# Kernel tuning notes

Measured on AMD Instinct MI355X. Metric: run time of the kernel, lower is better.

Reference implementation:

```python
import jax, jax.numpy as jnp
import numpy as np

GRID_SIZE = 5
SPLINE_ORDER = 3
GRID_RANGE = (-1.0, 1.0)
IN_FEATURES = 1024
OUT_FEATURES = 1024
NUM_BASIS = GRID_SIZE + SPLINE_ORDER  # 8
SCALE_BASE = 1.0
SCALE_SPLINE = 1.0

_h = (GRID_RANGE[1] - GRID_RANGE[0]) / GRID_SIZE
_GRID = np.linspace(GRID_RANGE[0] - SPLINE_ORDER * _h,
                    GRID_RANGE[1] + SPLINE_ORDER * _h,
                    GRID_SIZE + 2 * SPLINE_ORDER + 1).astype(np.float32)  # (12,)


def bspline_basis(x, grid):
    # x: (B, I)  ->  basis: (B, I, NUM_BASIS)
    x = jnp.clip(x, GRID_RANGE[0], GRID_RANGE[1])
    xg = x[..., None]                              # (B, I, 1)
    g = grid                                       # (G,) broadcasts over (B, I)
    basis = ((xg >= g[:-1]) & (xg < g[1:])).astype(x.dtype)  # (B, I, G-1)
    for k in range(1, SPLINE_ORDER + 1):
        left_den = g[k:-1] - g[:-(k + 1)]
        left_den = jnp.where(left_den == 0, jnp.ones_like(left_den), left_den)
        right_den = g[k + 1:] - g[1:-k]
        right_den = jnp.where(right_den == 0, jnp.ones_like(right_den), right_den)
        left = (xg - g[:-(k + 1)]) / left_den * basis[..., :-1]
        right = (g[k + 1:] - xg) / right_den * basis[..., 1:]
        basis = left + right
    return basis


def setup_inputs() -> dict:
    key = jax.random.key(0)
    k1, k2, k3 = jax.random.split(key, 3)
    x = jax.random.normal(k1, (8192, IN_FEATURES), dtype=jnp.float32)
    base_weight = jax.random.normal(k2, (OUT_FEATURES, IN_FEATURES), dtype=jnp.float32) * 0.03
    spline_weight = jax.random.normal(k3, (OUT_FEATURES, IN_FEATURES, NUM_BASIS), dtype=jnp.float32) * 0.03
    return {"x": x, "base_weight": base_weight, "spline_weight": spline_weight}


def reference(x, base_weight, spline_weight):
    grid = jnp.asarray(_GRID, dtype=x.dtype)
    # base branch: SiLU(x) @ W_base^T
    base_out = jax.nn.silu(x) @ base_weight.T              # (B, O)
    base_out = base_out * SCALE_BASE
    # spline branch: einsum over (in, basis)
    basis = bspline_basis(x, grid)                         # (B, I, K)
    spline_out = jnp.einsum('bik,oik->bo', basis, spline_weight)
    spline_out = spline_out * SCALE_SPLINE
    return base_out + spline_out
```

## Files before the change

kernel.cpp:

```cpp
#include <hip/hip_runtime.h>
#include <hip/hip_bf16.h>
#include <cstdint>


typedef short s16x8 __attribute__((ext_vector_type(8)));
typedef float f32x4 __attribute__((ext_vector_type(4)));

#define GK 9216
#define GN 1024
#define GI 1024
#define GM 8192

#define BS_BLK 32768
#define RP_BLK 4608

__device__ __forceinline__ void cp16(const __hip_bfloat16* g, __hip_bfloat16* l) {
  __builtin_amdgcn_global_load_lds((const __attribute__((address_space(1))) void*)g,
                                   (__attribute__((address_space(3))) void*)l, 16, 0, 0);
}

__device__ __forceinline__ uint32_t bfbits(float f) {
  __hip_bfloat16 h = __float2bfloat16(f);
  unsigned short us;
  __builtin_memcpy(&us, &h, 2);
  return (uint32_t)us;
}

__device__ __forceinline__ void basis4(float xv, int& jj, float& w0, float& w1,
                                       float& w2, float& w3) {
  float t = fminf(1.f, fmaxf(-1.f, xv));
  float us = (t + 1.f) * 2.5f;
  int j = (int)us;
  if (j > 4) j = 4;
  float u = us - (float)j;
  float u2 = u * u, u3 = u2 * u;
  float om = 1.f - u;
  jj = j;
  w0 = om * om * om * (1.f / 6.f);
  w1 = (3.f * u3 - 6.f * u2 + 4.f) * (1.f / 6.f);
  w2 = (-3.f * u3 + 3.f * u2 + 3.f * u + 1.f) * (1.f / 6.f);
  w3 = u3 * (1.f / 6.f);
}

__global__ void kan_prep_all(const float* __restrict__ x,
                             const float* __restrict__ baseW,
                             const float* __restrict__ splineW,
                             __hip_bfloat16* __restrict__ W2,
                             __hip_bfloat16* __restrict__ A) {
  int bid = blockIdx.x;
  if (bid < BS_BLK) {
    int t = bid * 256 + threadIdx.x;
    int b = t >> 10, i = t & 1023;
    float xv = x[t];

    float sl = xv / (1.f + __expf(-xv));
    A[(size_t)b * GK + 8192 + i] = __float2bfloat16(sl);

    int jj; float w0, w1, w2, w3;
    basis4(xv, jj, w0, w1, w2, w3);
    uint64_t W64 = (uint64_t)(bfbits(w0) | (bfbits(w1) << 16)) |
                   ((uint64_t)(bfbits(w2) | (bfbits(w3) << 16)) << 32);
    int sh = jj * 16;
    uint64_t lo = (jj < 4) ? (W64 << sh) : 0ull;
    uint64_t hi = (jj == 0) ? 0ull : (W64 >> (64 - sh));
    uint4 pk;
    pk.x = (uint32_t)lo;  pk.y = (uint32_t)(lo >> 32);
    pk.z = (uint32_t)hi;  pk.w = (uint32_t)(hi >> 32);
    *(uint4*)(A + (size_t)b * GK + (size_t)i * 8) = pk;
  } else {
    int t = (bid - BS_BLK) * 256 + threadIdx.x;
    int o = t / 1152;
    int c = (t - o * 1152) * 8;
    const float* src = (c < 8192) ? (splineW + (size_t)o * 8192 + c)
                                  : (baseW + (size_t)o * GI + (c - 8192));
    float4 v0 = ((const float4*)src)[0];
    float4 v1 = ((const float4*)src)[1];
    uint4 pk;
    pk.x = bfbits(v0.x) | (bfbits(v0.y) << 16);
    pk.y = bfbits(v0.z) | (bfbits(v0.w) << 16);
    pk.z = bfbits(v1.x) | (bfbits(v1.y) << 16);
    pk.w = bfbits(v1.z) | (bfbits(v1.w) << 16);
    *(uint4*)(W2 + (size_t)o * GK + c) = pk;
  }
}

__global__ __launch_bounds__(256) void kan_gemm(
    const __hip_bfloat16* __restrict__ A,
    const __hip_bfloat16* __restrict__ B,
    float* __restrict__ C) {
  __shared__ __align__(16) __hip_bfloat16 As[2][128 * 32];
  __shared__ __align__(16) __hip_bfloat16 Bs[2][128 * 32];
  const int tid = threadIdx.x;
  const int lane = tid & 63;
  const int wave = tid >> 6;
  const int wm = wave >> 1, wn = wave & 1;

  const int linear = blockIdx.y * 8 + blockIdx.x;
  const int rowBand = (linear & 7) * 8 + ((linear >> 3) & 7);
  const int colBand = linear >> 6;
  const int blockRow = rowBand * 128;
  const int blockCol = colBand * 128;

  const __hip_bfloat16* aPtr = A + (size_t)(blockRow + (tid >> 2)) * GK + (tid & 3) * 8;
  const __hip_bfloat16* bPtr = B + (size_t)(blockCol + (tid >> 2)) * GK + (tid & 3) * 8;
  __hip_bfloat16* ldsA0 = As[0] + wave * 512;
  __hip_bfloat16* ldsA1 = As[1] + wave * 512;
  __hip_bfloat16* ldsB0 = Bs[0] + wave * 512;
  __hip_bfloat16* ldsB1 = Bs[1] + wave * 512;

  f32x4 acc[4][4] = {};

  const int q = lane >> 4;
  const int r16 = lane & 15;
  const int aRow = wm * 64 + r16;
  const int bRow = wn * 64 + r16;

  for (int kt = 0; kt < GK / 64; ++kt) {
    cp16(aPtr, ldsA0);
    cp16(aPtr + (size_t)64 * GK, ldsA0 + 2048);
    cp16(aPtr + 32, ldsA1);
    cp16(aPtr + 32 + (size_t)64 * GK, ldsA1 + 2048);
    cp16(bPtr, ldsB0);
    cp16(bPtr + (size_t)64 * GK, ldsB0 + 2048);
    cp16(bPtr + 32, ldsB1);
    cp16(bPtr + 32 + (size_t)64 * GK, ldsB1 + 2048);
    aPtr += 64; bPtr += 64;
    __syncthreads();

#pragma unroll
    for (int s = 0; s < 2; ++s) {
      const s16x8* Af = (const s16x8*)As[s];
      const s16x8* Bf = (const s16x8*)Bs[s];
      s16x8 af[4], bfg[4];
#pragma unroll
      for (int tm = 0; tm < 4; ++tm) af[tm] = Af[(aRow + tm * 16) * 4 + q];
#pragma unroll
      for (int tn = 0; tn < 4; ++tn) bfg[tn] = Bf[(bRow + tn * 16) * 4 + q];
#pragma unroll
      for (int tm = 0; tm < 4; ++tm)
#pragma unroll
        for (int tn = 0; tn < 4; ++tn)
          acc[tm][tn] = __builtin_amdgcn_mfma_f32_16x16x32_bf16(
              af[tm], bfg[tn], acc[tm][tn], 0, 0, 0);
    }
    __syncthreads();
  }

  const int cRow0 = blockRow + wm * 64 + q * 4;
  const int cCol0 = blockCol + wn * 64 + r16;
#pragma unroll
  for (int tm = 0; tm < 4; ++tm)
#pragma unroll
    for (int tn = 0; tn < 4; ++tn) {
      int col = cCol0 + tn * 16;
#pragma unroll
      for (int r = 0; r < 4; ++r) {
        int row = cRow0 + tm * 16 + r;
        C[(size_t)row * GN + col] = acc[tm][tn][r];
      }
    }
}

__global__ void kan_naive(const float* __restrict__ x,
                          const float* __restrict__ bw,
                          const float* __restrict__ sw,
                          float* __restrict__ out) {
  int o = blockIdx.x * 256 + threadIdx.x;
  int b = blockIdx.y;
  float acc = 0.f;
  for (int i = 0; i < GI; ++i) {
    float xv = x[(size_t)b * GI + i];
    float sl = xv / (1.f + __expf(-xv));
    acc += sl * bw[(size_t)o * GI + i];
    int jj; float w0, w1, w2, w3;
    basis4(xv, jj, w0, w1, w2, w3);
    const float* swr = sw + ((size_t)o * GI + i) * 8 + jj;
    acc += w0 * swr[0] + w1 * swr[1] + w2 * swr[2] + w3 * swr[3];
  }
  out[(size_t)b * GN + o] = acc;
}

extern "C" void kernel_launch(void* const* d_in, const int* in_sizes, int n_in,
                              void* d_out, int out_size, void* d_ws, size_t ws_size,
                              hipStream_t stream) {
  const float* x  = (const float*)d_in[0];
  const float* bw = (const float*)d_in[1];
  const float* sw = (const float*)d_in[2];
  float* out = (float*)d_out;

  const size_t wBytes = (size_t)GK * GN * 2;
  const size_t aBytes = (size_t)GM * GK * 2;
  if (ws_size < wBytes + aBytes) {
    kan_naive<<<dim3(GN / 256, GM), 256, 0, stream>>>(x, bw, sw, out);
    return;
  }

  __hip_bfloat16* W2 = (__hip_bfloat16*)d_ws;
  __hip_bfloat16* Abuf = W2 + (size_t)GK * GN;

  kan_prep_all<<<BS_BLK + RP_BLK, 256, 0, stream>>>(x, bw, sw, W2, Abuf);
  kan_gemm<<<dim3(GN / 128, GM / 128), 256, 0, stream>>>(Abuf, W2, out);
}
```

Measured before the change: 290.0 us.

## Fuse prep and GEMM into one kernel with a global grid barrier

The separate preprocessing kernel (basis expansion, SiLU, weight conversion to bf16) is merged into the GEMM kernel. Each of the 512 GEMM blocks first prepares a slice of the activation and weight buffers, then waits at an atomic-counter grid barrier before running the matmul. This removes a kernel launch and its tail, but it relies on all 512 blocks being resident at once (launch_bounds 256,2), adds a memset, and makes the prep phase run with far fewer threads than before.

```diff
diff --git a/kernel.cpp b/kernel.cpp
--- a/kernel.cpp
+++ b/kernel.cpp
@@ -10,9 +10,7 @@
 #define GN 1024
 #define GI 1024
 #define GM 8192
-
-#define BS_BLK 32768
-#define RP_BLK 4608
+#define NBLOCKS 512u
 
 __device__ __forceinline__ void cp16(const __hip_bfloat16* g, __hip_bfloat16* l) {
   __builtin_amdgcn_global_load_lds((const __attribute__((address_space(1))) void*)g,
@@ -42,67 +40,96 @@
   w3 = u3 * (1.f / 6.f);
 }
 
-__global__ void kan_prep_all(const float* __restrict__ x,
-                             const float* __restrict__ baseW,
-                             const float* __restrict__ splineW,
-                             __hip_bfloat16* __restrict__ W2,
-                             __hip_bfloat16* __restrict__ A) {
-  int bid = blockIdx.x;
-  if (bid < BS_BLK) {
-    int t = bid * 256 + threadIdx.x;
-    int b = t >> 10, i = t & 1023;
-    float xv = x[t];
-
-    float sl = xv / (1.f + __expf(-xv));
-    A[(size_t)b * GK + 8192 + i] = __float2bfloat16(sl);
-
-    int jj; float w0, w1, w2, w3;
-    basis4(xv, jj, w0, w1, w2, w3);
-    uint64_t W64 = (uint64_t)(bfbits(w0) | (bfbits(w1) << 16)) |
-                   ((uint64_t)(bfbits(w2) | (bfbits(w3) << 16)) << 32);
-    int sh = jj * 16;
-    uint64_t lo = (jj < 4) ? (W64 << sh) : 0ull;
-    uint64_t hi = (jj == 0) ? 0ull : (W64 >> (64 - sh));
-    uint4 pk;
-    pk.x = (uint32_t)lo;  pk.y = (uint32_t)(lo >> 32);
-    pk.z = (uint32_t)hi;  pk.w = (uint32_t)(hi >> 32);
-    *(uint4*)(A + (size_t)b * GK + (size_t)i * 8) = pk;
-  } else {
-    int t = (bid - BS_BLK) * 256 + threadIdx.x;
-    int o = t / 1152;
-    int c = (t - o * 1152) * 8;
-    const float* src = (c < 8192) ? (splineW + (size_t)o * 8192 + c)
-                                  : (baseW + (size_t)o * GI + (c - 8192));
-    float4 v0 = ((const float4*)src)[0];
-    float4 v1 = ((const float4*)src)[1];
-    uint4 pk;
-    pk.x = bfbits(v0.x) | (bfbits(v0.y) << 16);
-    pk.y = bfbits(v0.z) | (bfbits(v0.w) << 16);
-    pk.z = bfbits(v1.x) | (bfbits(v1.y) << 16);
-    pk.w = bfbits(v1.z) | (bfbits(v1.w) << 16);
-    *(uint4*)(W2 + (size_t)o * GK + c) = pk;
-  }
-}
-
-__global__ __launch_bounds__(256) void kan_gemm(
-    const __hip_bfloat16* __restrict__ A,
-    const __hip_bfloat16* __restrict__ B,
-    float* __restrict__ C) {
+__device__ __forceinline__ uint4 basispack(float xv) {
+  int jj; float w0, w1, w2, w3;
+  basis4(xv, jj, w0, w1, w2, w3);
+  uint64_t W64 = (uint64_t)(bfbits(w0) | (bfbits(w1) << 16)) |
+                 ((uint64_t)(bfbits(w2) | (bfbits(w3) << 16)) << 32);
+  int sh = jj * 16;
+  uint64_t lo = (jj < 4) ? (W64 << sh) : 0ull;
+  uint64_t hi = (jj == 0) ? 0ull : (W64 >> (64 - sh));
+  uint4 pk;
+  pk.x = (uint32_t)lo;  pk.y = (uint32_t)(lo >> 32);
+  pk.z = (uint32_t)hi;  pk.w = (uint32_t)(hi >> 32);
+  return pk;
+}
+
+__global__ __launch_bounds__(256, 2) void kan_fused(
+    const float* __restrict__ x,
+    const float* __restrict__ baseW,
+    const float* __restrict__ splineW,
+    __hip_bfloat16* __restrict__ W2,
+    __hip_bfloat16* __restrict__ A,
+    float* __restrict__ C,
+    uint32_t* __restrict__ gate) {
   __shared__ __align__(16) __hip_bfloat16 As[2][128 * 32];
   __shared__ __align__(16) __hip_bfloat16 Bs[2][128 * 32];
   const int tid = threadIdx.x;
+
+  const int linear = blockIdx.y * 8 + blockIdx.x;
+  const int rowBand = (linear & 7) * 8 + ((linear >> 3) & 7);
+  const int colBand = linear >> 6;
+
+  {
+    const int rowStart = rowBand * 128 + colBand * 16;
+#pragma unroll 4
+    for (int it = 0; it < 16; ++it) {
+      int f = it * 1024 + tid * 4;
+      int b = rowStart + (f >> 10);
+      int i = f & 1023;
+      float4 xv = *(const float4*)(x + (size_t)b * GI + i);
+      uint4* bp = (uint4*)(A + (size_t)b * GK + (size_t)i * 8);
+      bp[0] = basispack(xv.x);
+      bp[1] = basispack(xv.y);
+      bp[2] = basispack(xv.z);
+      bp[3] = basispack(xv.w);
+      float s0 = xv.x / (1.f + __expf(-xv.x));
+      float s1 = xv.y / (1.f + __expf(-xv.y));
+      float s2 = xv.z / (1.f + __expf(-xv.z));
+      float s3 = xv.w / (1.f + __expf(-xv.w));
+      uint2 sp;
+      sp.x = bfbits(s0) | (bfbits(s1) << 16);
+      sp.y = bfbits(s2) | (bfbits(s3) << 16);
+      *(uint2*)(A + (size_t)b * GK + 8192 + i) = sp;
+    }
+  }
+
+  {
+#pragma unroll
+    for (int k = 0; k < 9; ++k) {
+      int chunk = k * 256 + tid;
+      int o = linear * 2 + (chunk / 1152);
+      int c = (chunk % 1152) * 8;
+      const float* src = (c < 8192) ? (splineW + (size_t)o * 8192 + c)
+                                    : (baseW + (size_t)o * GI + (c - 8192));
+      float4 v0 = ((const float4*)src)[0];
+      float4 v1 = ((const float4*)src)[1];
+      uint4 pk;
+      pk.x = bfbits(v0.x) | (bfbits(v0.y) << 16);
+      pk.y = bfbits(v0.z) | (bfbits(v0.w) << 16);
+      pk.z = bfbits(v1.x) | (bfbits(v1.y) << 16);
+      pk.w = bfbits(v1.z) | (bfbits(v1.w) << 16);
+      *(uint4*)(W2 + (size_t)o * GK + c) = pk;
+    }
+  }
+
+  __syncthreads();
+  if (tid == 0) {
+    __threadfence();
+    atomicAdd(gate, 1u);
+    while (atomicAdd(gate, 0u) < NBLOCKS) __builtin_amdgcn_s_sleep(2);
+  }
+  __syncthreads();
+  __threadfence();
+
   const int lane = tid & 63;
   const int wave = tid >> 6;
   const int wm = wave >> 1, wn = wave & 1;
-
-  const int linear = blockIdx.y * 8 + blockIdx.x;
-  const int rowBand = (linear & 7) * 8 + ((linear >> 3) & 7);
-  const int colBand = linear >> 6;
   const int blockRow = rowBand * 128;
   const int blockCol = colBand * 128;
 
   const __hip_bfloat16* aPtr = A + (size_t)(blockRow + (tid >> 2)) * GK + (tid & 3) * 8;
-  const __hip_bfloat16* bPtr = B + (size_t)(blockCol + (tid >> 2)) * GK + (tid & 3) * 8;
+  const __hip_bfloat16* bPtr = W2 + (size_t)(blockCol + (tid >> 2)) * GK + (tid & 3) * 8;
   __hip_bfloat16* ldsA0 = As[0] + wave * 512;
   __hip_bfloat16* ldsA1 = As[1] + wave * 512;
   __hip_bfloat16* ldsB0 = Bs[0] + wave * 512;
@@ -190,14 +217,16 @@
 
   const size_t wBytes = (size_t)GK * GN * 2;
   const size_t aBytes = (size_t)GM * GK * 2;
-  if (ws_size < wBytes + aBytes) {
+  if (ws_size < wBytes + aBytes + 64) {
     kan_naive<<<dim3(GN / 256, GM), 256, 0, stream>>>(x, bw, sw, out);
     return;
   }
 
   __hip_bfloat16* W2 = (__hip_bfloat16*)d_ws;
   __hip_bfloat16* Abuf = W2 + (size_t)GK * GN;
-
-  kan_prep_all<<<BS_BLK + RP_BLK, 256, 0, stream>>>(x, bw, sw, W2, Abuf);
-  kan_gemm<<<dim3(GN / 128, GM / 128), 256, 0, stream>>>(Abuf, W2, out);
-}
+  uint32_t* gate = (uint32_t*)((char*)d_ws + wBytes + aBytes);
+
+  hipMemsetAsync(gate, 0, sizeof(uint32_t), stream);
+  kan_fused<<<dim3(GN / 128, GM / 128), 256, 0, stream>>>(
+      x, bw, sw, W2, Abuf, out, gate);
+}
```

After: 401.9 us. +38.6%, slower.
